# Kernel tuning notes

Hardware: AMD Instinct MI355X
Metric: run time of the kernel (lower is better)

## Reference

```python
import jax, jax.numpy as jnp
import numpy as np

DIST_THRESH = 2.5


def _level_losses(lvl_cls, lvl_reg, gt_boxes, gt_labels):
    # lvl_cls: [B, HW, nc], lvl_reg: [B, HW, 4], gt_boxes: [B, N, 4], gt_labels: [B, N]
    gt_xy = gt_boxes[..., :2]            # [B, N, 2]
    pred_xy = lvl_reg[..., :2]           # [B, HW, 2]
    # squared euclidean distances [B, N, HW] (cdist equivalent; min/argmin unaffected by sqrt)
    d2 = jnp.sum((gt_xy[:, :, None, :] - pred_xy[:, None, :, :]) ** 2, axis=-1)
    min_d2 = jnp.min(d2, axis=2)         # [B, N]
    matches = jnp.argmin(d2, axis=2)     # [B, N]
    valid = jnp.sqrt(min_d2) < DIST_THRESH  # [B, N] bool
    # gather matched predictions per gt
    g_cls = jnp.take_along_axis(lvl_cls, matches[..., None], axis=1)   # [B, N, nc]
    g_reg = jnp.take_along_axis(lvl_reg, matches[..., None], axis=1)   # [B, N, 4]
    # cross entropy (reduction='none'), summed over valid matches
    logp = jax.nn.log_softmax(g_cls, axis=-1)
    ce = -jnp.take_along_axis(logp, gt_labels[..., None], axis=-1)[..., 0]  # [B, N]
    l1 = jnp.abs(g_reg - gt_boxes).sum(axis=-1)                             # [B, N]
    w = valid.astype(lvl_cls.dtype)
    return (ce * w).sum(), (l1 * w).sum(), w.sum()


def setup_inputs() -> dict:
    key = jax.random.key(0)
    ks = jax.random.split(key, 8)
    B, N, nc = 16, 128, 80
    hws = [25600, 6400, 1600]
    inp = {}
    for i, hw in enumerate(hws):
        inp[f"pred_cls_{i}"] = jax.random.normal(ks[i], (B, hw, nc), dtype=jnp.float32)
        inp[f"pred_reg_{i}"] = jax.random.normal(ks[3 + i], (B, hw, 4), dtype=jnp.float32)
    inp["gt_boxes"] = jax.random.normal(ks[6], (B, N, 4), dtype=jnp.float32)
    inp["gt_labels"] = jax.random.randint(ks[7], (B, N), 0, nc)
    return inp


def reference(pred_cls_0, pred_cls_1, pred_cls_2,
              pred_reg_0, pred_reg_1, pred_reg_2,
              gt_boxes, gt_labels):
    cls_list = [pred_cls_0, pred_cls_1, pred_cls_2]
    reg_list = [pred_reg_0, pred_reg_1, pred_reg_2]
    cls_loss = jnp.zeros((), jnp.float32)
    reg_loss = jnp.zeros((), jnp.float32)
    num_pos = jnp.zeros((), jnp.float32)
    for lvl_cls, lvl_reg in zip(cls_list, reg_list):
        c, r, n = _level_losses(lvl_cls, lvl_reg, gt_boxes, gt_labels)
        cls_loss = cls_loss + c
        reg_loss = reg_loss + r
        num_pos = num_pos + n
    denom = jnp.maximum(num_pos, 1.0)
    return cls_loss / denom, reg_loss / denom, num_pos
```

## Files before the change

### kernel.cpp

```cpp
#include <hip/hip_runtime.h>
#include <cstdint>
#include <cstddef>

#define NTH 256
#define NGT 128
#define BATCH 16
#define NC 80
#define G 16
#define NCHUNK (NGT / G)
#define HW0 25600
#define HW1 6400
#define HW2 1600
#define SL0 4
#define MAXSL 4
#define NLOSS_BLK (3 * BATCH * NGT / 4)

#define PART_OFF   0
#define PART_BYTES (3 * BATCH * NGT * MAXSL * 8)
#define PARTL_OFF  PART_BYTES
#define PARTL_BYTES (NLOSS_BLK * 3 * (int)sizeof(float))
#define CNT_OFF    (PARTL_OFF + PARTL_BYTES)

__device__ __forceinline__ unsigned long long umin64(unsigned long long a, unsigned long long b) {
    return a < b ? a : b;
}

#define EVAL(px, py, idx_) do {                                                   \
    _Pragma("unroll")                                                             \
    for (int g = 0; g < G; ++g) {                                                 \
        float dx = gx[g] - (px), dy = gy[g] - (py);                               \
        float d2 = dx * dx + dy * dy;                                             \
        unsigned long long key =                                                  \
            ((unsigned long long)__float_as_uint(d2) << 32) | (unsigned)(idx_);   \
        kmin[g] = umin64(kmin[g], key);                                           \
    } } while (0)

__global__ __launch_bounds__(NTH) void scan_kernel(
    const float4* __restrict__ reg0, const float4* __restrict__ reg1, const float4* __restrict__ reg2,
    const float* __restrict__ gt_boxes,
    unsigned long long* __restrict__ part, unsigned int* __restrict__ counter)
{
    if (blockIdx.x == 0 && threadIdx.x == 0) *counter = 0u;

    int x = blockIdx.x;
    int lvl, b, slice, chunk, HW, nsl;
    const float4* src;
    if (x < BATCH * SL0 * NCHUNK) {
        lvl = 0; b = x / (SL0 * NCHUNK);
        int r = x % (SL0 * NCHUNK);
        slice = r / NCHUNK; chunk = r % NCHUNK;
        HW = HW0; nsl = SL0; src = reg0;
    } else if (x < BATCH * SL0 * NCHUNK + BATCH * NCHUNK) {
        int y = x - BATCH * SL0 * NCHUNK;
        lvl = 1; b = y / NCHUNK; chunk = y % NCHUNK; slice = 0;
        HW = HW1; nsl = 1; src = reg1;
    } else {
        int y = x - BATCH * SL0 * NCHUNK - BATCH * NCHUNK;
        lvl = 2; b = y / NCHUNK; chunk = y % NCHUNK; slice = 0;
        HW = HW2; nsl = 1; src = reg2;
    }

    const int seg = HW / nsl;
    const int e0 = slice * seg, e1 = e0 + seg;
    const int tid = threadIdx.x, wave = tid >> 6, lane = tid & 63;
    const int n0 = chunk * G;

    float gx[G], gy[G];
#pragma unroll
    for (int g = 0; g < G; ++g) {
        const float* gb = gt_boxes + (size_t)(b * NGT + n0 + g) * 4;
        gx[g] = gb[0]; gy[g] = gb[1];
    }

    unsigned long long kmin[G];
#pragma unroll
    for (int g = 0; g < G; ++g) kmin[g] = ~0ull;

    const float4* base = src + (size_t)b * HW;
    for (int i = e0 + tid; i < e1; i += NTH) {
        float4 p = base[i];
        EVAL(p.x, p.y, i);
    }

#pragma unroll
    for (int g = 0; g < G; ++g) {
#pragma unroll
        for (int off = 32; off >= 1; off >>= 1) {
            unsigned long long o = __shfl_down(kmin[g], off, 64);
            kmin[g] = umin64(kmin[g], o);
        }
    }

    __shared__ unsigned long long smem[G][4];
    if (lane == 0) {
#pragma unroll
        for (int g = 0; g < G; ++g) smem[g][wave] = kmin[g];
    }
    __syncthreads();

    if (tid < G) {
        unsigned long long key = umin64(umin64(smem[tid][0], smem[tid][1]),
                                        umin64(smem[tid][2], smem[tid][3]));
        part[((size_t)(lvl * BATCH + b) * NGT + n0 + tid) * MAXSL + slice] = key;
    }
}

__global__ __launch_bounds__(NTH) void loss_kernel(
    const float* __restrict__ cls0, const float* __restrict__ cls1, const float* __restrict__ cls2,
    const float* __restrict__ reg0, const float* __restrict__ reg1, const float* __restrict__ reg2,
    const float* __restrict__ gt_boxes, const int* __restrict__ gt_labels,
    const unsigned long long* __restrict__ part, float* __restrict__ partl,
    unsigned int* __restrict__ counter, float* __restrict__ out)
{
    const int wave = threadIdx.x >> 6;
    const int lane = threadIdx.x & 63;
    const int gid = blockIdx.x * 4 + wave;
    const int lvl = gid / (BATCH * NGT);
    const int r = gid % (BATCH * NGT);
    const int b = r / NGT, n = r % NGT;

    const float* cls; const float* reg; int HW, S;
    if (lvl == 0)      { cls = cls0; reg = reg0; HW = HW0; S = SL0; }
    else if (lvl == 1) { cls = cls1; reg = reg1; HW = HW1; S = 1; }
    else               { cls = cls2; reg = reg2; HW = HW2; S = 1; }

    const unsigned long long* p = part + (size_t)gid * MAXSL;
    unsigned long long key = p[0];
    for (int s = 1; s < S; ++s) key = umin64(key, p[s]);

    int match = (int)(unsigned)(key & 0xffffffffu);
    float d2min = __uint_as_float((unsigned)(key >> 32));
    bool valid = d2min < 6.25f;

    const int label = gt_labels[b * NGT + n];
    const float* c = cls + ((size_t)b * HW + match) * NC;

    float x1 = c[lane];
    float x2 = (lane < NC - 64) ? c[64 + lane] : -INFINITY;
    float mx = fmaxf(x1, x2);
#pragma unroll
    for (int off = 32; off >= 1; off >>= 1) mx = fmaxf(mx, __shfl_xor(mx, off, 64));
    float s = expf(x1 - mx) + ((lane < NC - 64) ? expf(x2 - mx) : 0.0f);
#pragma unroll
    for (int off = 32; off >= 1; off >>= 1) s += __shfl_xor(s, off, 64);

    __shared__ float ce_s[4], l1_s[4], w_s[4];
    __shared__ int is_last;
    if (lane == 0) {
        float ce = 0.0f, l1 = 0.0f, w = 0.0f;
        if (valid) {
            float xlab = c[label];
            ce = -(xlab - mx - logf(s));
            const float* gb = gt_boxes + (size_t)(b * NGT + n) * 4;
            const float* gr = reg + ((size_t)b * HW + match) * 4;
            l1 = fabsf(gr[0] - gb[0]) + fabsf(gr[1] - gb[1]) +
                 fabsf(gr[2] - gb[2]) + fabsf(gr[3] - gb[3]);
            w = 1.0f;
        }
        ce_s[wave] = ce; l1_s[wave] = l1; w_s[wave] = w;
    }
    __syncthreads();

    if (threadIdx.x == 0) {
        float* o = partl + (size_t)blockIdx.x * 3;
        o[0] = ce_s[0] + ce_s[1] + ce_s[2] + ce_s[3];
        o[1] = l1_s[0] + l1_s[1] + l1_s[2] + l1_s[3];
        o[2] = w_s[0] + w_s[1] + w_s[2] + w_s[3];
        __threadfence();
        unsigned int old = atomicAdd(counter, 1u);
        is_last = (old == (unsigned)(NLOSS_BLK - 1));
    }
    __syncthreads();

    if (is_last) {
        __threadfence();
        const int tid = threadIdx.x;
        float ce = 0.0f, l1 = 0.0f, w = 0.0f;
        for (int i = tid; i < NLOSS_BLK; i += NTH) {
            ce += partl[(size_t)i * 3 + 0];
            l1 += partl[(size_t)i * 3 + 1];
            w  += partl[(size_t)i * 3 + 2];
        }
#pragma unroll
        for (int off = 32; off >= 1; off >>= 1) {
            ce += __shfl_xor(ce, off, 64);
            l1 += __shfl_xor(l1, off, 64);
            w  += __shfl_xor(w,  off, 64);
        }
        __shared__ float sm[3][4];
        if (lane == 0) { sm[0][wave] = ce; sm[1][wave] = l1; sm[2][wave] = w; }
        __syncthreads();
        if (tid == 0) {
            float tce = sm[0][0] + sm[0][1] + sm[0][2] + sm[0][3];
            float tl1 = sm[1][0] + sm[1][1] + sm[1][2] + sm[1][3];
            float tw  = sm[2][0] + sm[2][1] + sm[2][2] + sm[2][3];
            float denom = fmaxf(tw, 1.0f);
            out[0] = tce / denom;
            out[1] = tl1 / denom;
            out[2] = tw;
        }
    }
}

extern "C" void kernel_launch(void* const* d_in, const int* in_sizes, int n_in,
                              void* d_out, int out_size, void* d_ws, size_t ws_size,
                              hipStream_t stream) {
    const float* cls0 = nullptr; const float* cls1 = nullptr; const float* cls2 = nullptr;
    const float* reg0 = nullptr; const float* reg1 = nullptr; const float* reg2 = nullptr;
    const float* gt_boxes = nullptr; const int* gt_labels = nullptr;
    for (int i = 0; i < n_in; ++i) {
        switch (in_sizes[i]) {
            case BATCH * HW0 * NC: cls0 = (const float*)d_in[i]; break;
            case BATCH * HW1 * NC: cls1 = (const float*)d_in[i]; break;
            case BATCH * HW2 * NC: cls2 = (const float*)d_in[i]; break;
            case BATCH * HW0 * 4:  reg0 = (const float*)d_in[i]; break;
            case BATCH * HW1 * 4:  reg1 = (const float*)d_in[i]; break;
            case BATCH * HW2 * 4:  reg2 = (const float*)d_in[i]; break;
            case BATCH * NGT * 4:  gt_boxes = (const float*)d_in[i]; break;
            case BATCH * NGT:      gt_labels = (const int*)d_in[i]; break;
            default: break;
        }
    }

    char* ws = (char*)d_ws;
    unsigned long long* part = (unsigned long long*)(ws + PART_OFF);
    float* partl = (float*)(ws + PARTL_OFF);
    unsigned int* counter = (unsigned int*)(ws + CNT_OFF);

    const int scan_grid = BATCH * SL0 * NCHUNK + 2 * BATCH * NCHUNK;
    scan_kernel<<<scan_grid, NTH, 0, stream>>>(
        (const float4*)reg0, (const float4*)reg1, (const float4*)reg2,
        gt_boxes, part, counter);

    loss_kernel<<<NLOSS_BLK, NTH, 0, stream>>>(
        cls0, cls1, cls2, reg0, reg1, reg2, gt_boxes, gt_labels,
        part, partl, counter, (float*)d_out);
}
```

Baseline: 248.0 us.

## Fuse nearest-match scan with loss computation and drop level-0 slicing

```diff
diff --git a/kernel.cpp b/kernel.cpp
--- a/kernel.cpp
+++ b/kernel.cpp
@@ -11,15 +11,7 @@
 #define HW0 25600
 #define HW1 6400
 #define HW2 1600
-#define SL0 4
-#define MAXSL 4
-#define NLOSS_BLK (3 * BATCH * NGT / 4)
-
-#define PART_OFF   0
-#define PART_BYTES (3 * BATCH * NGT * MAXSL * 8)
-#define PARTL_OFF  PART_BYTES
-#define PARTL_BYTES (NLOSS_BLK * 3 * (int)sizeof(float))
-#define CNT_OFF    (PARTL_OFF + PARTL_BYTES)
+#define NBLK (3 * BATCH * NCHUNK)
 
 __device__ __forceinline__ unsigned long long umin64(unsigned long long a, unsigned long long b) {
     return a < b ? a : b;
@@ -35,33 +27,22 @@
         kmin[g] = umin64(kmin[g], key);                                           \
     } } while (0)
 
-__global__ __launch_bounds__(NTH) void scan_kernel(
-    const float4* __restrict__ reg0, const float4* __restrict__ reg1, const float4* __restrict__ reg2,
-    const float* __restrict__ gt_boxes,
-    unsigned long long* __restrict__ part, unsigned int* __restrict__ counter)
+__global__ __launch_bounds__(NTH) void scan_loss_kernel(
+    const float* __restrict__ cls0, const float* __restrict__ cls1, const float* __restrict__ cls2,
+    const float* __restrict__ reg0, const float* __restrict__ reg1, const float* __restrict__ reg2,
+    const float* __restrict__ gt_boxes, const int* __restrict__ gt_labels,
+    float* __restrict__ partl)
 {
-    if (blockIdx.x == 0 && threadIdx.x == 0) *counter = 0u;
+    const int x = blockIdx.x;
+    const int lvl = x >> 7;
+    const int y = x & 127;
+    const int b = y >> 3, chunk = y & 7;
 
-    int x = blockIdx.x;
-    int lvl, b, slice, chunk, HW, nsl;
-    const float4* src;
-    if (x < BATCH * SL0 * NCHUNK) {
-        lvl = 0; b = x / (SL0 * NCHUNK);
-        int r = x % (SL0 * NCHUNK);
-        slice = r / NCHUNK; chunk = r % NCHUNK;
-        HW = HW0; nsl = SL0; src = reg0;
-    } else if (x < BATCH * SL0 * NCHUNK + BATCH * NCHUNK) {
-        int y = x - BATCH * SL0 * NCHUNK;
-        lvl = 1; b = y / NCHUNK; chunk = y % NCHUNK; slice = 0;
-        HW = HW1; nsl = 1; src = reg1;
-    } else {
-        int y = x - BATCH * SL0 * NCHUNK - BATCH * NCHUNK;
-        lvl = 2; b = y / NCHUNK; chunk = y % NCHUNK; slice = 0;
-        HW = HW2; nsl = 1; src = reg2;
-    }
+    const float* cls; const float* reg; int HW;
+    if (lvl == 0)      { cls = cls0; reg = reg0; HW = HW0; }
+    else if (lvl == 1) { cls = cls1; reg = reg1; HW = HW1; }
+    else               { cls = cls2; reg = reg2; HW = HW2; }
 
-    const int seg = HW / nsl;
-    const int e0 = slice * seg, e1 = e0 + seg;
     const int tid = threadIdx.x, wave = tid >> 6, lane = tid & 63;
     const int n0 = chunk * G;
 
@@ -76,8 +57,8 @@
 #pragma unroll
     for (int g = 0; g < G; ++g) kmin[g] = ~0ull;
 
-    const float4* base = src + (size_t)b * HW;
-    for (int i = e0 + tid; i < e1; i += NTH) {
+    const float4* base = reinterpret_cast<const float4*>(reg) + (size_t)b * HW;
+    for (int i = tid; i < HW; i += NTH) {
         float4 p = base[i];
         EVAL(p.x, p.y, i);
     }
@@ -98,107 +79,85 @@
     }
     __syncthreads();
 
+    __shared__ unsigned long long keyf[G];
     if (tid < G) {
-        unsigned long long key = umin64(umin64(smem[tid][0], smem[tid][1]),
-                                        umin64(smem[tid][2], smem[tid][3]));
-        part[((size_t)(lvl * BATCH + b) * NGT + n0 + tid) * MAXSL + slice] = key;
+        keyf[tid] = umin64(umin64(smem[tid][0], smem[tid][1]),
+                           umin64(smem[tid][2], smem[tid][3]));
+    }
+    __syncthreads();
+
+    float ce_acc = 0.0f, l1_acc = 0.0f, w_acc = 0.0f;
+#pragma unroll
+    for (int j = 0; j < 4; ++j) {
+        const int g = wave * 4 + j;
+        unsigned long long key = keyf[g];
+        int match = (int)(unsigned)(key & 0xffffffffu);
+        float d2min = __uint_as_float((unsigned)(key >> 32));
+        bool valid = d2min < 6.25f;
+        if (!valid) continue;
+
+        const int n = n0 + g;
+        const int label = gt_labels[b * NGT + n];
+        const float* c = cls + ((size_t)b * HW + match) * NC;
+
+        float x1 = c[lane];
+        float x2 = (lane < NC - 64) ? c[64 + lane] : -INFINITY;
+        float mx = fmaxf(x1, x2);
+#pragma unroll
+        for (int off = 32; off >= 1; off >>= 1) mx = fmaxf(mx, __shfl_xor(mx, off, 64));
+        float s = expf(x1 - mx) + ((lane < NC - 64) ? expf(x2 - mx) : 0.0f);
+#pragma unroll
+        for (int off = 32; off >= 1; off >>= 1) s += __shfl_xor(s, off, 64);
+
+        if (lane == 0) {
+            ce_acc += -(c[label] - mx - logf(s));
+            const float* gb = gt_boxes + (size_t)(b * NGT + n) * 4;
+            const float* gr = reg + ((size_t)b * HW + match) * 4;
+            l1_acc += fabsf(gr[0] - gb[0]) + fabsf(gr[1] - gb[1]) +
+                      fabsf(gr[2] - gb[2]) + fabsf(gr[3] - gb[3]);
+            w_acc += 1.0f;
+        }
+    }
+
+    __shared__ float cw[4][3];
+    if (lane == 0) { cw[wave][0] = ce_acc; cw[wave][1] = l1_acc; cw[wave][2] = w_acc; }
+    __syncthreads();
+
+    if (tid == 0) {
+        float* o = partl + (size_t)blockIdx.x * 3;
+        o[0] = cw[0][0] + cw[1][0] + cw[2][0] + cw[3][0];
+        o[1] = cw[0][1] + cw[1][1] + cw[2][1] + cw[3][1];
+        o[2] = cw[0][2] + cw[1][2] + cw[2][2] + cw[3][2];
     }
 }
 
-__global__ __launch_bounds__(NTH) void loss_kernel(
-    const float* __restrict__ cls0, const float* __restrict__ cls1, const float* __restrict__ cls2,
-    const float* __restrict__ reg0, const float* __restrict__ reg1, const float* __restrict__ reg2,
-    const float* __restrict__ gt_boxes, const int* __restrict__ gt_labels,
-    const unsigned long long* __restrict__ part, float* __restrict__ partl,
-    unsigned int* __restrict__ counter, float* __restrict__ out)
+__global__ __launch_bounds__(NTH) void finalize_kernel(
+    const float* __restrict__ partl, float* __restrict__ out)
 {
-    const int wave = threadIdx.x >> 6;
-    const int lane = threadIdx.x & 63;
-    const int gid = blockIdx.x * 4 + wave;
-    const int lvl = gid / (BATCH * NGT);
-    const int r = gid % (BATCH * NGT);
-    const int b = r / NGT, n = r % NGT;
-
-    const float* cls; const float* reg; int HW, S;
-    if (lvl == 0)      { cls = cls0; reg = reg0; HW = HW0; S = SL0; }
-    else if (lvl == 1) { cls = cls1; reg = reg1; HW = HW1; S = 1; }
-    else               { cls = cls2; reg = reg2; HW = HW2; S = 1; }
-
-    const unsigned long long* p = part + (size_t)gid * MAXSL;
-    unsigned long long key = p[0];
-    for (int s = 1; s < S; ++s) key = umin64(key, p[s]);
-
-    int match = (int)(unsigned)(key & 0xffffffffu);
-    float d2min = __uint_as_float((unsigned)(key >> 32));
-    bool valid = d2min < 6.25f;
-
-    const int label = gt_labels[b * NGT + n];
-    const float* c = cls + ((size_t)b * HW + match) * NC;
-
-    float x1 = c[lane];
-    float x2 = (lane < NC - 64) ? c[64 + lane] : -INFINITY;
-    float mx = fmaxf(x1, x2);
+    const int tid = threadIdx.x, wave = tid >> 6, lane = tid & 63;
+    float ce = 0.0f, l1 = 0.0f, w = 0.0f;
+    for (int i = tid; i < NBLK; i += NTH) {
+        ce += partl[(size_t)i * 3 + 0];
+        l1 += partl[(size_t)i * 3 + 1];
+        w  += partl[(size_t)i * 3 + 2];
+    }
 #pragma unroll
-    for (int off = 32; off >= 1; off >>= 1) mx = fmaxf(mx, __shfl_xor(mx, off, 64));
-    float s = expf(x1 - mx) + ((lane < NC - 64) ? expf(x2 - mx) : 0.0f);
-#pragma unroll
-    for (int off = 32; off >= 1; off >>= 1) s += __shfl_xor(s, off, 64);
-
-    __shared__ float ce_s[4], l1_s[4], w_s[4];
-    __shared__ int is_last;
-    if (lane == 0) {
-        float ce = 0.0f, l1 = 0.0f, w = 0.0f;
-        if (valid) {
-            float xlab = c[label];
-            ce = -(xlab - mx - logf(s));
-            const float* gb = gt_boxes + (size_t)(b * NGT + n) * 4;
-            const float* gr = reg + ((size_t)b * HW + match) * 4;
-            l1 = fabsf(gr[0] - gb[0]) + fabsf(gr[1] - gb[1]) +
-                 fabsf(gr[2] - gb[2]) + fabsf(gr[3] - gb[3]);
-            w = 1.0f;
-        }
-        ce_s[wave] = ce; l1_s[wave] = l1; w_s[wave] = w;
+    for (int off = 32; off >= 1; off >>= 1) {
+        ce += __shfl_xor(ce, off, 64);
+        l1 += __shfl_xor(l1, off, 64);
+        w  += __shfl_xor(w,  off, 64);
     }
+    __shared__ float sm[3][4];
+    if (lane == 0) { sm[0][wave] = ce; sm[1][wave] = l1; sm[2][wave] = w; }
     __syncthreads();
-
-    if (threadIdx.x == 0) {
-        float* o = partl + (size_t)blockIdx.x * 3;
-        o[0] = ce_s[0] + ce_s[1] + ce_s[2] + ce_s[3];
-        o[1] = l1_s[0] + l1_s[1] + l1_s[2] + l1_s[3];
-        o[2] = w_s[0] + w_s[1] + w_s[2] + w_s[3];
-        __threadfence();
-        unsigned int old = atomicAdd(counter, 1u);
-        is_last = (old == (unsigned)(NLOSS_BLK - 1));
-    }
-    __syncthreads();
-
-    if (is_last) {
-        __threadfence();
-        const int tid = threadIdx.x;
-        float ce = 0.0f, l1 = 0.0f, w = 0.0f;
-        for (int i = tid; i < NLOSS_BLK; i += NTH) {
-            ce += partl[(size_t)i * 3 + 0];
-            l1 += partl[(size_t)i * 3 + 1];
-            w  += partl[(size_t)i * 3 + 2];
-        }
-#pragma unroll
-        for (int off = 32; off >= 1; off >>= 1) {
-            ce += __shfl_xor(ce, off, 64);
-            l1 += __shfl_xor(l1, off, 64);
-            w  += __shfl_xor(w,  off, 64);
-        }
-        __shared__ float sm[3][4];
-        if (lane == 0) { sm[0][wave] = ce; sm[1][wave] = l1; sm[2][wave] = w; }
-        __syncthreads();
-        if (tid == 0) {
-            float tce = sm[0][0] + sm[0][1] + sm[0][2] + sm[0][3];
-            float tl1 = sm[1][0] + sm[1][1] + sm[1][2] + sm[1][3];
-            float tw  = sm[2][0] + sm[2][1] + sm[2][2] + sm[2][3];
-            float denom = fmaxf(tw, 1.0f);
-            out[0] = tce / denom;
-            out[1] = tl1 / denom;
-            out[2] = tw;
-        }
+    if (tid == 0) {
+        float tce = sm[0][0] + sm[0][1] + sm[0][2] + sm[0][3];
+        float tl1 = sm[1][0] + sm[1][1] + sm[1][2] + sm[1][3];
+        float tw  = sm[2][0] + sm[2][1] + sm[2][2] + sm[2][3];
+        float denom = fmaxf(tw, 1.0f);
+        out[0] = tce / denom;
+        out[1] = tl1 / denom;
+        out[2] = tw;
     }
 }
 
@@ -222,17 +181,10 @@
         }
     }
 
-    char* ws = (char*)d_ws;
-    unsigned long long* part = (unsigned long long*)(ws + PART_OFF);
-    float* partl = (float*)(ws + PARTL_OFF);
-    unsigned int* counter = (unsigned int*)(ws + CNT_OFF);
+    float* partl = (float*)d_ws;
 
-    const int scan_grid = BATCH * SL0 * NCHUNK + 2 * BATCH * NCHUNK;
-    scan_kernel<<<scan_grid, NTH, 0, stream>>>(
-        (const float4*)reg0, (const float4*)reg1, (const float4*)reg2,
-        gt_boxes, part, counter);
+    scan_loss_kernel<<<NBLK, NTH, 0, stream>>>(
+        cls0, cls1, cls2, reg0, reg1, reg2, gt_boxes, gt_labels, partl);
 
-    loss_kernel<<<NLOSS_BLK, NTH, 0, stream>>>(
-        cls0, cls1, cls2, reg0, reg1, reg2, gt_boxes, gt_labels,
-        part, partl, counter, (float*)d_out);
+    finalize_kernel<<<1, NTH, 0, stream>>>(partl, (float*)d_out);
 }
```

Result: slower. 267.3 us (+7.8%).
